# Kernel optimization log

Measured on AMD Instinct MI355X. Metric: run time of the kernel, lower is better.

Reference implementation:

```python
import jax, jax.numpy as jnp
import numpy as np

B, T, D, H = 4, 2048, 1024, 8
HD = D // H  # head_dim = 128


def setup_inputs() -> dict:
    key = jax.random.key(0)
    ks = jax.random.split(key, 10)
    s = 1.0 / np.sqrt(D)
    return {
        "x": jax.random.normal(ks[0], (B, T, D), jnp.float32),
        "y": jax.random.normal(ks[1], (B, T, D), jnp.float32),
        "Wq": jax.random.normal(ks[2], (D, D), jnp.float32) * s,
        "bq": jnp.zeros((D,), jnp.float32),
        "Wk": jax.random.normal(ks[3], (D, D), jnp.float32) * s,
        "bk": jnp.zeros((D,), jnp.float32),
        "Wv": jax.random.normal(ks[4], (D, D), jnp.float32) * s,
        "bv": jnp.zeros((D,), jnp.float32),
        "Wo": jax.random.normal(ks[5], (D, D), jnp.float32) * s,
        "bo": jnp.zeros((D,), jnp.float32),
    }


def _heads(t):
    # [B, T, D] -> [B, H, T, HD]
    b, t_, _ = t.shape
    return t.reshape(b, t_, H, HD).transpose(0, 2, 1, 3)


def reference(x, y, Wq, bq, Wk, bk, Wv, bv, Wo, bo):
    Tq, Tk = x.shape[1], y.shape[1]
    q = _heads(x @ Wq.T + bq)  # [B,H,Tq,HD]
    k = _heads(y @ Wk.T + bk)  # [B,H,Tk,HD]
    v = _heads(y @ Wv.T + bv)  # [B,H,Tk,HD]
    scale = 1.0 / np.sqrt(HD)
    logits = jnp.einsum("bhqd,bhkd->bhqk", q, k) * scale
    # causal mask: positions k > q get -inf
    causal = jnp.triu(jnp.full((Tq, Tk), -jnp.inf, jnp.float32), k=1)
    logits = logits + causal
    attn = jax.nn.softmax(logits, axis=-1)  # [B,H,Tq,Tk]
    ctx = jnp.einsum("bhqk,bhkd->bhqd", attn, v)
    ctx = ctx.transpose(0, 2, 1, 3).reshape(x.shape[0], Tq, D)
    out = ctx @ Wo.T + bo
    return out
```

## Files before the change

kernel.cpp:

```cpp
#include <hip/hip_runtime.h>
#include <math.h>

#define TB 4
#define TT 2048
#define TD 1024
#define TH 8
#define THD 128

typedef __attribute__((ext_vector_type(8))) short short8;
typedef __attribute__((ext_vector_type(4))) short short4v;
typedef __attribute__((ext_vector_type(4))) float float4v;
typedef __attribute__((ext_vector_type(16))) float float16v;

__device__ __forceinline__ short f2bf(float f) {
    union { float f; unsigned u; } v; v.f = f;
    unsigned r = v.u + 0x7FFFu + ((v.u >> 16) & 1u);
    return (short)(r >> 16);
}

__device__ __forceinline__ float bf2f(short s) {
    union { unsigned u; float f; } v;
    v.u = ((unsigned)(unsigned short)s) << 16;
    return v.f;
}

__device__ __forceinline__ short8 cvt8(float4v a, float4v b) {
    short8 r;
    r[0] = f2bf(a[0]); r[1] = f2bf(a[1]); r[2] = f2bf(a[2]); r[3] = f2bf(a[3]);
    r[4] = f2bf(b[0]); r[5] = f2bf(b[1]); r[6] = f2bf(b[2]); r[7] = f2bf(b[3]);
    return r;
}

__device__ __forceinline__ void async16(const void* g, void* l) {
    __builtin_amdgcn_global_load_lds(
        (const __attribute__((address_space(1))) unsigned int*)g,
        (__attribute__((address_space(3))) unsigned int*)l, 16, 0, 0);
}

__global__ void cvtall(const float* __restrict__ x, const float* __restrict__ y,
                       const float* __restrict__ wq, const float* __restrict__ wk,
                       const float* __restrict__ wv, const float* __restrict__ wo,
                       short* __restrict__ xyb, short* __restrict__ wb)
{
    const size_t SZ = (size_t)TB * TT * TD;
    const size_t WSZ = (size_t)TD * TD;
    const int bid = blockIdx.x;
    const float* s; short* d; size_t base;
    if (bid < 8192) {
        int ty = bid >> 12;
        s = ty ? y : x;
        d = xyb + (size_t)ty * SZ;
        base = (size_t)(bid & 4095) * 2048;
    } else {
        int wi = bid - 8192;
        int w = wi >> 9;
        s = (w == 0) ? wq : (w == 1) ? wk : (w == 2) ? wv : wo;
        d = wb + (size_t)w * WSZ;
        base = (size_t)(wi & 511) * 2048;
    }
    size_t i = base + (size_t)threadIdx.x * 8;
    float4v v0 = *(const float4v*)(s + i);
    float4v v1 = *(const float4v*)(s + i + 4);
    *(short8*)(d + i) = cvt8(v0, v1);
}

__device__ __forceinline__ void gemm_core256(const short* __restrict__ A,
                                             const short* __restrict__ W,
                                             int m0, int n0, short* SM,
                                             float4v acc[4][4])
{
    short* As = SM;
    short* Bs = SM + 32768;
    const int tid = threadIdx.x;
    const int lane = tid & 63, wid = tid >> 6;
    const int lr = lane & 15, qd = lane >> 4, sw = lane & 7;
    const int wr = wid >> 1, wc = wid & 1;
    const int rsub = lane >> 3;
    const int gj = ((lane & 7) ^ rsub) * 8;
    const int K = TD;

    const short* aSrc[4]; int aDst[4];
    const short* bSrc[2]; int bDst[2];
#pragma unroll
    for (int p = 0; p < 4; ++p) {
        int ch = wid * 4 + p;
        aSrc[p] = A + (size_t)(m0 + ch * 8 + rsub) * K + gj;
        aDst[p] = ch * 512;
    }
#pragma unroll
    for (int p = 0; p < 2; ++p) {
        int ch = wid * 2 + p;
        bSrc[p] = W + (size_t)(n0 + ch * 8 + rsub) * K + gj;
        bDst[p] = ch * 512;
    }

#pragma unroll
    for (int mt = 0; mt < 4; ++mt)
#pragma unroll
        for (int nt = 0; nt < 4; ++nt)
            acc[mt][nt] = float4v{0.f, 0.f, 0.f, 0.f};

#pragma unroll
    for (int t = 0; t < 2; ++t) {
#pragma unroll
        for (int p = 0; p < 4; ++p)
            async16(aSrc[p] + t * 64, As + t * 16384 + aDst[p]);
#pragma unroll
        for (int p = 0; p < 2; ++p)
            async16(bSrc[p] + t * 64, Bs + t * 8192 + bDst[p]);
    }
    asm volatile("s_waitcnt vmcnt(6)" ::: "memory");
    __builtin_amdgcn_sched_barrier(0);
    __builtin_amdgcn_s_barrier();

#pragma unroll 2
    for (int it = 0; it < 16; ++it) {
        const short* Ac = As + (it & 1) * 16384;
        const short* Bc = Bs + (it & 1) * 8192;
        short* Asn = As + (it & 1) * 16384;
        short* Bsn = Bs + (it & 1) * 8192;
        const int kb2 = (it + 2) * 64;
        const bool stg = (it < 14);

        short8 af[4][2], bf[4][2];

#pragma unroll
        for (int mi = 0; mi < 4; ++mi)
#pragma unroll
            for (int ks = 0; ks < 2; ++ks)
                af[mi][ks] = *(const short8*)&Ac[(wr * 64 + mi * 16 + lr) * 64 +
                                                 (((ks * 4 + qd) ^ sw) * 8)];
#pragma unroll
        for (int ni = 0; ni < 2; ++ni)
#pragma unroll
            for (int ks = 0; ks < 2; ++ks)
                bf[ni][ks] = *(const short8*)&Bc[(wc * 64 + ni * 16 + lr) * 64 +
                                                 (((ks * 4 + qd) ^ sw) * 8)];
        __builtin_amdgcn_sched_barrier(0);
#pragma unroll
        for (int ni = 2; ni < 4; ++ni)
#pragma unroll
            for (int ks = 0; ks < 2; ++ks)
                bf[ni][ks] = *(const short8*)&Bc[(wc * 64 + ni * 16 + lr) * 64 +
                                                 (((ks * 4 + qd) ^ sw) * 8)];
        asm volatile("s_waitcnt lgkmcnt(4)" ::: "memory");
        __builtin_amdgcn_sched_barrier(0);
        __builtin_amdgcn_s_setprio(1);
#pragma unroll
        for (int mi = 0; mi < 4; ++mi)
#pragma unroll
            for (int ni = 0; ni < 2; ++ni)
#pragma unroll
                for (int ks = 0; ks < 2; ++ks)
                    acc[mi][ni] = __builtin_amdgcn_mfma_f32_16x16x32_bf16(
                        af[mi][ks], bf[ni][ks], acc[mi][ni], 0, 0, 0);
        __builtin_amdgcn_s_setprio(0);
        __builtin_amdgcn_sched_barrier(0);
        asm volatile("s_waitcnt lgkmcnt(0)" ::: "memory");
        __builtin_amdgcn_sched_barrier(0);
        __builtin_amdgcn_s_barrier();
        __builtin_amdgcn_sched_barrier(0);

        if (stg) {
#pragma unroll
            for (int p = 0; p < 4; ++p)
                async16(aSrc[p] + kb2, Asn + aDst[p]);
#pragma unroll
            for (int p = 0; p < 2; ++p)
                async16(bSrc[p] + kb2, Bsn + bDst[p]);
        }
        __builtin_amdgcn_s_setprio(1);
#pragma unroll
        for (int mi = 0; mi < 4; ++mi)
#pragma unroll
            for (int ni = 2; ni < 4; ++ni)
#pragma unroll
                for (int ks = 0; ks < 2; ++ks)
                    acc[mi][ni] = __builtin_amdgcn_mfma_f32_16x16x32_bf16(
                        af[mi][ks], bf[ni][ks], acc[mi][ni], 0, 0, 0);
        __builtin_amdgcn_s_setprio(0);
        if (stg) { asm volatile("s_waitcnt vmcnt(6)" ::: "memory"); }
        else     { asm volatile("s_waitcnt vmcnt(0)" ::: "memory"); }
        __builtin_amdgcn_sched_barrier(0);
        __builtin_amdgcn_s_barrier();
    }
}

__global__ __launch_bounds__(512, 2)
void gemm_qkv8(const short* __restrict__ xyb, const short* __restrict__ wb,
               const float* __restrict__ bq, const float* __restrict__ bk,
               const float* __restrict__ bv,
               short* __restrict__ qhp, short* __restrict__ khp,
               short* __restrict__ vtp)
{
    __shared__ __attribute__((aligned(16))) short SM[49152];
    const size_t SZ = (size_t)TB * TT * TD;
    const int bid = blockIdx.x;
    const int lin = (bid & 7) * 96 + (bid >> 3);
    const int by = lin / 24, bx = lin - by * 24;
    const int mode = bx >> 3;
    const int n0 = (bx & 7) * 128;
    const int h_ = n0 >> 7;
    const int m0 = by * 256;
    const short* A = (mode == 0) ? xyb : (xyb + SZ);
    const short* W = wb + (size_t)mode * TD * TD;
    const float* bias = (mode == 0) ? bq : (mode == 1) ? bk : bv;
    const float scale = (mode == 0)
        ? (0.08838834764831845f * 1.4426950408889634f) : 1.0f;

    float4v acc[4][4];
    gemm_core256(A, W, m0, n0, SM, acc);

    const int tid = threadIdx.x;
    const int lane = tid & 63, wid = tid >> 6;
    const int lr = lane & 15, qd = lane >> 4;
    const int wr = wid >> 1, wc = wid & 1;

#pragma unroll
    for (int nt = 0; nt < 4; ++nt) {
        int col = wc * 64 + nt * 16 + lr;
        float bi = bias[n0 + col];
#pragma unroll
        for (int mt = 0; mt < 4; ++mt)
#pragma unroll
            for (int i = 0; i < 4; ++i) {
                int row = wr * 64 + mt * 16 + qd * 4 + i;
                short v = f2bf((acc[mt][nt][i] + bi) * scale);
                if (mode < 2) SM[row * 128 + col] = v;
                else          SM[col * 264 + row] = v;
            }
    }
    __syncthreads();

    if (mode < 2) {
        short* outp = (mode == 0) ? qhp : khp;
#pragma unroll
        for (int r8 = 0; r8 < 8; ++r8) {
            int row = r8 * 32 + (tid >> 4), c = tid & 15;
            short8 v = *(const short8*)&SM[row * 128 + c * 8];
            int tg = m0 + row;
            int b_ = tg >> 11, t_ = tg & (TT - 1);
            *(short8*)&outp[(((size_t)(b_ * TH + h_)) * TT + t_) * THD + c * 8] = v;
        }
    } else {
        int b_ = m0 >> 11, t0 = m0 & (TT - 1);
#pragma unroll
        for (int r8 = 0; r8 < 8; ++r8) {
            int hd = r8 * 16 + (tid >> 5), c = tid & 31;
            short8 v = *(const short8*)&SM[hd * 264 + c * 8];
            *(short8*)&vtp[(((size_t)(b_ * TH + h_)) * THD + hd) * TT + t0 + c * 8] = v;
        }
    }
}

__global__ __launch_bounds__(512, 2)
void gemm_out8(const short* __restrict__ A, const short* __restrict__ W,
               const float* __restrict__ bias, float* __restrict__ outp)
{
    __shared__ __attribute__((aligned(16))) short SM[49152];
    const int bid = blockIdx.x;
    const int lin = (bid & 7) * 32 + (bid >> 3);
    const int by = lin >> 3, bx = lin & 7;
    const int m0 = by * 256, n0 = bx * 128;

    float4v acc[4][4];
    gemm_core256(A, W, m0, n0, SM, acc);

    const int tid = threadIdx.x;
    const int lane = tid & 63, wid = tid >> 6;
    const int lr = lane & 15, qd = lane >> 4;
    const int wr = wid >> 1, wc = wid & 1;
#pragma unroll
    for (int nt = 0; nt < 4; ++nt) {
        int col = n0 + wc * 64 + nt * 16 + lr;
        float bi = bias[col];
#pragma unroll
        for (int mt = 0; mt < 4; ++mt)
#pragma unroll
            for (int i = 0; i < 4; ++i) {
                int row = m0 + wr * 64 + mt * 16 + qd * 4 + i;
                outp[(size_t)row * TD + col] = acc[mt][nt][i] + bi;
            }
    }
}

__global__ __launch_bounds__(256, 2)
void attn_fwd(const short* __restrict__ qh, const short* __restrict__ kh,
              const short* __restrict__ vt, short* __restrict__ po,
              float* __restrict__ pl)
{
    __shared__ __attribute__((aligned(16))) short Ks[2][64 * 128];
    __shared__ __attribute__((aligned(16))) short Vs[2][128 * 64];

    const int tid = threadIdx.x;
    const int lane = tid & 63, wid = tid >> 6;
    const int l31 = lane & 31, h = lane >> 5;
    const int sw7 = l31 & 7;

    const int bi = blockIdx.x;
    const int bh = bi & 31;
    const int j  = bi >> 5;
    const size_t bho = (size_t)bh * TT * THD;

    for (int u = 0; u < 2; ++u) {
        const int qt  = u ? (15 - j) : j;
        const int kv0 = u ? (qt + 1) : 0;
        const int kv1 = u ? (2 * qt + 2) : (j + 1);

        short8 qf[8];
        {
            const short* qp = qh + bho + (size_t)(qt * 128 + wid * 32 + l31) * THD;
#pragma unroll
            for (int ks = 0; ks < 8; ++ks)
                qf[ks] = *(const short8*)(qp + ks * 16 + h * 8);
        }
        float16v o[4];
#pragma unroll
        for (int db = 0; db < 4; ++db)
#pragma unroll
            for (int r = 0; r < 16; ++r) o[db][r] = 0.f;
        float li = 0.f;

        {
            const short* kbase = kh + bho + (size_t)kv0 * 64 * THD;
            const short* vbase = vt + (size_t)bh * THD * TT + (size_t)kv0 * 64;
#pragma unroll
            for (int p = 0; p < 4; ++p) {
                int ch = wid * 4 + p;
                int kr = ch * 4 + (lane >> 4);
                int kg = (lane & 15) ^ (kr & 7);
                async16(kbase + (size_t)kr * THD + kg * 8, &Ks[0][ch * 512]);
                int vr = ch * 8 + (lane >> 3);
                int vg = (lane & 7) ^ (vr & 7);
                async16(vbase + (size_t)vr * TT + vg * 8, &Vs[0][ch * 512]);
            }
        }
        __syncthreads();

        int cur = 0;
        for (int kv = kv0; kv < kv1; ++kv) {
            if (kv + 1 < kv1) {
                const short* kbase = kh + bho + (size_t)(kv + 1) * 64 * THD;
                const short* vbase = vt + (size_t)bh * THD * TT +
                                     (size_t)(kv + 1) * 64;
#pragma unroll
                for (int p = 0; p < 4; ++p) {
                    int ch = wid * 4 + p;
                    int kr = ch * 4 + (lane >> 4);
                    int kg = (lane & 15) ^ (kr & 7);
                    async16(kbase + (size_t)kr * THD + kg * 8,
                            &Ks[cur ^ 1][ch * 512]);
                    int vr = ch * 8 + (lane >> 3);
                    int vg = (lane & 7) ^ (vr & 7);
                    async16(vbase + (size_t)vr * TT + vg * 8,
                            &Vs[cur ^ 1][ch * 512]);
                }
            }

            const short* Kc = Ks[cur];
            const short* Vc = Vs[cur];

            float16v s[2];
#pragma unroll
            for (int kb = 0; kb < 2; ++kb)
#pragma unroll
                for (int r = 0; r < 16; ++r) s[kb][r] = 0.f;
#pragma unroll
            for (int ks = 0; ks < 8; ++ks) {
                int cidx = ((ks * 2 + h) ^ sw7) * 8;
                short8 kf0 = *(const short8*)&Kc[l31 * 128 + cidx];
                short8 kf1 = *(const short8*)&Kc[(32 + l31) * 128 + cidx];
                s[0] = __builtin_amdgcn_mfma_f32_32x32x16_bf16(kf0, qf[ks], s[0], 0, 0, 0);
                s[1] = __builtin_amdgcn_mfma_f32_32x32x16_bf16(kf1, qf[ks], s[1], 0, 0, 0);
            }

            if (kv >= 2 * qt) {
                int q = qt * 128 + wid * 32 + l31;
#pragma unroll
                for (int r = 0; r < 16; ++r) {
                    int key = kv * 64 + (r & 3) + 8 * (r >> 2) + 4 * h;
                    if (key > q) s[0][r] = -1e30f;
                    if (key + 32 > q) s[1][r] = -1e30f;
                }
            }

#pragma unroll
            for (int st = 0; st < 8; ++st) {
                float e0 = exp2f(s[st >> 2][(st & 3) * 4 + 0]);
                float e1 = exp2f(s[st >> 2][(st & 3) * 4 + 1]);
                float e2 = exp2f(s[st >> 2][(st & 3) * 4 + 2]);
                float e3 = exp2f(s[st >> 2][(st & 3) * 4 + 3]);
                li += (e0 + e1) + (e2 + e3);
                short4v ap;
                ap[0] = f2bf(e0); ap[1] = f2bf(e1);
                ap[2] = f2bf(e2); ap[3] = f2bf(e3);
#pragma unroll
                for (int db = 0; db < 4; ++db) {
                    short4v vf = *(const short4v*)&Vc[(db * 32 + l31) * 64 +
                                                      ((st ^ sw7) * 8) + h * 4];
                    o[db] = __builtin_amdgcn_mfma_f32_32x32x8bf16_1k(ap, vf, o[db], 0, 0, 0);
                }
            }
            __syncthreads();
            cur ^= 1;
        }

        li += __shfl_xor(li, 32);
        const int slot = (bh * 16 + qt) * 2 + u;
        if (h == 0) pl[slot * 128 + wid * 32 + l31] = li;
        short* pop = po + (size_t)slot * 16384 + (size_t)(wid * 32) * 128 + l31;
#pragma unroll
        for (int r = 0; r < 16; ++r) {
            int ql = (r & 3) + 8 * (r >> 2) + 4 * h;
#pragma unroll
            for (int db = 0; db < 4; ++db)
                pop[(size_t)ql * 128 + db * 32] = f2bf(o[db][r]);
        }
    }
}

__global__ __launch_bounds__(256)
void combine(const short* __restrict__ po, const float* __restrict__ pl,
             short* __restrict__ ctx)
{
    const unsigned i = blockIdx.x * 256 + threadIdx.x;
    const int hdv = i & 15;
    const int q   = (i >> 4) & 127;
    const int qt  = (i >> 11) & 15;
    const int bh  = i >> 15;
    const int tile = bh * 16 + qt;
    const size_t base = (size_t)tile * 2 * 16384 + (size_t)q * 128 + hdv * 8;
    short8 a = *(const short8*)&po[base];
    short8 b = *(const short8*)&po[base + 16384];
    const float inv = 1.f / (pl[tile * 2 * 128 + q] + pl[(tile * 2 + 1) * 128 + q]);
    short8 r;
#pragma unroll
    for (int k = 0; k < 8; ++k)
        r[k] = f2bf((bf2f(a[k]) + bf2f(b[k])) * inv);
    const int b_ = bh >> 3, h_ = bh & 7, t = qt * 128 + q;
    *(short8*)&ctx[((size_t)(b_ * TT + t)) * TD + h_ * THD + hdv * 8] = r;
}

extern "C" void kernel_launch(void* const* d_in, const int* in_sizes, int n_in,
                              void* d_out, int out_size, void* d_ws, size_t ws_size,
                              hipStream_t stream) {
    (void)in_sizes; (void)n_in; (void)out_size; (void)ws_size;
    const float* x  = (const float*)d_in[0];
    const float* y  = (const float*)d_in[1];
    const float* Wq = (const float*)d_in[2];
    const float* bq = (const float*)d_in[3];
    const float* Wk = (const float*)d_in[4];
    const float* bk = (const float*)d_in[5];
    const float* Wv = (const float*)d_in[6];
    const float* bv = (const float*)d_in[7];
    const float* Wo = (const float*)d_in[8];
    const float* bo = (const float*)d_in[9];
    float* out = (float*)d_out;

    const size_t SZ = (size_t)TB * TT * TD;
    const size_t WSZ = (size_t)TD * TD;
    short* xyb = (short*)d_ws;
    short* wb  = xyb + 2 * SZ;
    short* qh  = wb + 4 * WSZ;
    short* kh  = qh + SZ;
    short* vt  = kh + SZ;
    float* pl  = (float*)(vt + SZ);
    short* po  = xyb;
    short* ctx = qh;

    hipLaunchKernelGGL(cvtall, dim3(10240), dim3(256), 0, stream,
                       x, y, Wq, Wk, Wv, Wo, xyb, wb);
    hipLaunchKernelGGL(gemm_qkv8, dim3(768), dim3(512), 0, stream,
                       xyb, wb, bq, bk, bv, qh, kh, vt);
    hipLaunchKernelGGL(attn_fwd, dim3(512), dim3(256), 0, stream, qh, kh, vt, po, pl);
    hipLaunchKernelGGL(combine, dim3(4096), dim3(256), 0, stream, po, pl, ctx);
    hipLaunchKernelGGL(gemm_out8, dim3(256), dim3(512), 0, stream,
                       ctx, wb + 3 * WSZ, bo, out);
}
```

Measured before the change: 282.8 us.

## Fuse split-KV combine into attention via atomic tile flags; use packed bf16 convert

Removes the separate combine kernel. Each attention block that finishes one half of a query tile bumps an atomic counter, and the second finisher merges both partial outputs and writes the normalized ctx directly. The flags are zeroed by an extra block in the conversion kernel, and the fused path only runs when the workspace is large enough. It also replaces the scalar float-to-bf16 conversions of the probabilities with packed v_cvt_pk_bf16_f32 instructions. The cost is extra fences, syncthreads and a device-wide dependency between blocks, plus a larger workspace requirement.

After: 464.7 us. 64.3% more time.

```diff
diff --git a/kernel.cpp b/kernel.cpp
--- a/kernel.cpp
+++ b/kernel.cpp
@@ -40,11 +40,19 @@
 __global__ void cvtall(const float* __restrict__ x, const float* __restrict__ y,
                        const float* __restrict__ wq, const float* __restrict__ wk,
                        const float* __restrict__ wv, const float* __restrict__ wo,
-                       short* __restrict__ xyb, short* __restrict__ wb)
+                       short* __restrict__ xyb, short* __restrict__ wb,
+                       int* __restrict__ flags)
 {
     const size_t SZ = (size_t)TB * TT * TD;
     const size_t WSZ = (size_t)TD * TD;
     const int bid = blockIdx.x;
+    if (bid >= 10240) {
+        if (flags) {
+            flags[threadIdx.x] = 0;
+            flags[threadIdx.x + 256] = 0;
+        }
+        return;
+    }
     const float* s; short* d; size_t base;
     if (bid < 8192) {
         int ty = bid >> 12;
@@ -287,10 +295,12 @@
 __global__ __launch_bounds__(256, 2)
 void attn_fwd(const short* __restrict__ qh, const short* __restrict__ kh,
               const short* __restrict__ vt, short* __restrict__ po,
-              float* __restrict__ pl)
+              float* __restrict__ pl, int* __restrict__ flags,
+              short* __restrict__ ctx)
 {
     __shared__ __attribute__((aligned(16))) short Ks[2][64 * 128];
     __shared__ __attribute__((aligned(16))) short Vs[2][128 * 64];
+    __shared__ int s_old;
 
     const int tid = threadIdx.x;
     const int lane = tid & 63, wid = tid >> 6;
@@ -391,9 +401,12 @@
                 float e2 = exp2f(s[st >> 2][(st & 3) * 4 + 2]);
                 float e3 = exp2f(s[st >> 2][(st & 3) * 4 + 3]);
                 li += (e0 + e1) + (e2 + e3);
-                short4v ap;
-                ap[0] = f2bf(e0); ap[1] = f2bf(e1);
-                ap[2] = f2bf(e2); ap[3] = f2bf(e3);
+                unsigned p0, p1;
+                asm("v_cvt_pk_bf16_f32 %0, %1, %2" : "=v"(p0) : "v"(e0), "v"(e1));
+                asm("v_cvt_pk_bf16_f32 %0, %1, %2" : "=v"(p1) : "v"(e2), "v"(e3));
+                union { unsigned u[2]; short4v s4; } pk;
+                pk.u[0] = p0; pk.u[1] = p1;
+                const short4v ap = pk.s4;
 #pragma unroll
                 for (int db = 0; db < 4; ++db) {
                     short4v vf = *(const short4v*)&Vc[(db * 32 + l31) * 64 +
@@ -415,6 +428,36 @@
 #pragma unroll
             for (int db = 0; db < 4; ++db)
                 pop[(size_t)ql * 128 + db * 32] = f2bf(o[db][r]);
+        }
+
+        if (flags) {
+            const int tile = bh * 16 + qt;
+            __threadfence();
+            __syncthreads();
+            if (tid == 0) s_old = atomicAdd(&flags[tile], 1);
+            __syncthreads();
+            if (s_old == 1) {
+                __threadfence();
+                const int oslot = tile * 2 + (1 - u);
+                const short* opo = po + (size_t)oslot * 16384;
+                const float* opl = pl + (size_t)oslot * 128;
+                const int b_ = bh >> 3, h_ = bh & 7;
+                short* cb = ctx + ((size_t)(b_ * TT + qt * 128 + wid * 32)) * TD
+                            + (size_t)h_ * THD + l31;
+#pragma unroll
+                for (int r = 0; r < 16; ++r) {
+                    int ql = (r & 3) + 8 * (r >> 2) + 4 * h;
+                    float lq = __shfl(li, ql, 32);
+                    float inv = 1.f / (lq + opl[wid * 32 + ql]);
+                    const short* ob = opo + (size_t)(wid * 32 + ql) * 128 + l31;
+                    short* cp = cb + (size_t)ql * TD;
+#pragma unroll
+                    for (int db = 0; db < 4; ++db)
+                        cp[db * 32] = f2bf((o[db][r] + bf2f(ob[db * 32])) * inv);
+                }
+                __syncthreads();
+                if (tid == 0) flags[tile] = 0;
+            }
         }
     }
 }
@@ -444,7 +487,7 @@
 extern "C" void kernel_launch(void* const* d_in, const int* in_sizes, int n_in,
                               void* d_out, int out_size, void* d_ws, size_t ws_size,
                               hipStream_t stream) {
-    (void)in_sizes; (void)n_in; (void)out_size; (void)ws_size;
+    (void)in_sizes; (void)n_in; (void)out_size;
     const float* x  = (const float*)d_in[0];
     const float* y  = (const float*)d_in[1];
     const float* Wq = (const float*)d_in[2];
@@ -465,15 +508,23 @@
     short* kh  = qh + SZ;
     short* vt  = kh + SZ;
     float* pl  = (float*)(vt + SZ);
+    int* flagp = (int*)(pl + 1024 * 128);
+    short* ctxf = (short*)(flagp + 512);
     short* po  = xyb;
-    short* ctx = qh;
-
-    hipLaunchKernelGGL(cvtall, dim3(10240), dim3(256), 0, stream,
-                       x, y, Wq, Wk, Wv, Wo, xyb, wb);
+
+    const size_t need = (size_t)(6 * SZ + 4 * WSZ) * 2
+                        + 1024 * 128 * 4 + 512 * 4 + SZ * 2;
+    const bool fused = (ws_size >= need);
+    short* ctx = fused ? ctxf : qh;
+
+    hipLaunchKernelGGL(cvtall, dim3(fused ? 10241 : 10240), dim3(256), 0, stream,
+                       x, y, Wq, Wk, Wv, Wo, xyb, wb, fused ? flagp : nullptr);
     hipLaunchKernelGGL(gemm_qkv8, dim3(768), dim3(512), 0, stream,
                        xyb, wb, bq, bk, bv, qh, kh, vt);
-    hipLaunchKernelGGL(attn_fwd, dim3(512), dim3(256), 0, stream, qh, kh, vt, po, pl);
-    hipLaunchKernelGGL(combine, dim3(4096), dim3(256), 0, stream, po, pl, ctx);
+    hipLaunchKernelGGL(attn_fwd, dim3(512), dim3(256), 0, stream,
+                       qh, kh, vt, po, pl, fused ? flagp : nullptr, ctx);
+    if (!fused)
+        hipLaunchKernelGGL(combine, dim3(4096), dim3(256), 0, stream, po, pl, ctx);
     hipLaunchKernelGGL(gemm_out8, dim3(256), dim3(512), 0, stream,
                        ctx, wb + 3 * WSZ, bo, out);
 }
```
